# Optimization experiments

Measured on AMD Instinct MI355X. Metric: run time of the kernel, lower is better.

## Reference

```python
import jax, jax.numpy as jnp
import numpy as np

D_MODEL = 1024
HEADS = 16
HEAD_DIM = D_MODEL // HEADS


def setup_inputs() -> dict:
    key = jax.random.key(0)
    k_x, k_q, k_k, k_v, k_o = jax.random.split(key, 5)
    x = jax.random.normal(k_x, (4, 2048, D_MODEL), dtype=jnp.float32)
    W_q = jax.random.normal(k_q, (D_MODEL, D_MODEL), dtype=jnp.float32)
    W_k = jax.random.normal(k_k, (D_MODEL, D_MODEL), dtype=jnp.float32)
    W_v = jax.random.normal(k_v, (D_MODEL, D_MODEL), dtype=jnp.float32)
    fc_out = jax.random.normal(k_o, (D_MODEL, D_MODEL), dtype=jnp.float32)
    return {"x": x, "W_q": W_q, "W_k": W_k, "W_v": W_v, "fc_out": fc_out}


def reference(x, W_q, W_k, W_v, fc_out):
    b, s, d = x.shape
    h, hd = HEADS, HEAD_DIM
    # Projections: [b, s, d]
    Q = x @ W_q
    K = x @ W_k
    V = x @ W_v
    # Split heads: [b, h, s, hd]
    Q = Q.reshape(b, s, h, hd).transpose(0, 2, 1, 3)
    K = K.reshape(b, s, h, hd).transpose(0, 2, 1, 3)
    V = V.reshape(b, s, h, hd).transpose(0, 2, 1, 3)
    # Scaled dot-product attention (softmax over key axis, per row)
    scores = jnp.einsum('bhqd,bhkd->bhqk', Q, K) / jnp.sqrt(jnp.float32(hd))
    attn = jax.nn.softmax(scores, axis=-1)
    head_out = jnp.einsum('bhqk,bhkd->bhqd', attn, V)
    # Concat heads back: [b, s, d]
    concat = head_out.transpose(0, 2, 1, 3).reshape(b, s, d)
    return concat @ fc_out
```

## Files before the change

### kernel.cpp

```cpp
#include <hip/hip_runtime.h>
#include <hip/hip_fp16.h>

#define BATCH   4
#define SEQ     2048
#define DM      1024
#define HEADS   16
#define HD      64
#define M_TOK   (BATCH * SEQ)
#define QK_LD   2048

#define QSCALE  0.1803368801111204f

typedef __attribute__((ext_vector_type(8)))  _Float16 half8;
typedef __attribute__((ext_vector_type(4)))  float    f32x4;
typedef __attribute__((ext_vector_type(16))) float    f32x16;

__device__ __forceinline__ unsigned short f2h(float x) {
    return __half_as_ushort(__float2half(x));
}
__device__ __forceinline__ float h2f(unsigned short u) {
    return __half2float(__ushort_as_half(u));
}
__device__ __forceinline__ float fast_exp2(float x) {
    float r; asm volatile("v_exp_f32 %0, %1" : "=v"(r) : "v"(x)); return r;
}
__device__ __forceinline__ unsigned int pk2(float a, float b) {
    __fp16 __attribute__((ext_vector_type(2))) h =
        __builtin_amdgcn_cvt_pkrtz(a, b);
    return __builtin_bit_cast(unsigned int, h);
}
__device__ __forceinline__ void dma16(const void* g, void* l) {
    __builtin_amdgcn_global_load_lds(
        (const __attribute__((address_space(1))) void*)g,
        (__attribute__((address_space(3))) void*)l, 16, 0, 0);
}

__global__ __launch_bounds__(256) void split_cast(
    const float* __restrict__ x, unsigned short* __restrict__ hi,
    unsigned short* __restrict__ lo)
{
    const int i = (blockIdx.x * 256 + threadIdx.x) * 8;
    float4 a = *(const float4*)(x + i);
    float4 b = *(const float4*)(x + i + 4);
    float v[8] = {a.x, a.y, a.z, a.w, b.x, b.y, b.z, b.w};
    unsigned short hb[8], lb[8];
#pragma unroll
    for (int j = 0; j < 8; ++j) {
        hb[j] = f2h(v[j]);
        lb[j] = f2h(v[j] - h2f(hb[j]));
    }
    *(float4*)(hi + i) = *(float4*)hb;
    *(float4*)(lo + i) = *(float4*)lb;
}

template<int SPLIT>
__global__ __launch_bounds__(256) void wtrans(
    const float* __restrict__ W, unsigned short* __restrict__ Th_out,
    unsigned short* __restrict__ Tl_out, float scale)
{
    __shared__ unsigned short Th[64][72];
    __shared__ unsigned short Tl[SPLIT ? 64 : 1][72];
    const int t  = threadIdx.x;
    const int n0 = blockIdx.x * 64, k0 = blockIdx.y * 64;
    const int kr = t >> 2, cg = (t & 3) << 4;
#pragma unroll
    for (int jj = 0; jj < 16; jj += 4) {
        float4 wv = *(const float4*)(W + (size_t)(k0 + kr) * DM + n0 + cg + jj);
        float vv[4] = {wv.x, wv.y, wv.z, wv.w};
#pragma unroll
        for (int j = 0; j < 4; ++j) {
            float v = vv[j] * scale;
            unsigned short h = f2h(v);
            Th[cg + jj + j][kr] = h;
            if (SPLIT) Tl[cg + jj + j][kr] = f2h(v - h2f(h));
        }
    }
    __syncthreads();
    const int nr = t >> 2, kg = (t & 3) << 4;
    size_t go = (size_t)(n0 + nr) * DM + k0 + kg;
    *(float4*)(Th_out + go)     = *(float4*)&Th[nr][kg];
    *(float4*)(Th_out + go + 8) = *(float4*)&Th[nr][kg + 8];
    if (SPLIT) {
        *(float4*)(Tl_out + go)     = *(float4*)&Tl[nr][kg];
        *(float4*)(Tl_out + go + 8) = *(float4*)&Tl[nr][kg + 8];
    }
}

template<int PASSES, int EPI>
__global__ __launch_bounds__(256, 2) void gemm_f16(
    const unsigned short* __restrict__ Ah, const unsigned short* __restrict__ Al,
    const unsigned short* __restrict__ Bh, const unsigned short* __restrict__ Bl,
    void* __restrict__ O0, void* __restrict__ O1, int M, int N, int K)
{
    __shared__ unsigned short As_h[128 * 32];
    __shared__ unsigned short Bs_h[128 * 32];
    __shared__ unsigned short As_l[PASSES == 3 ? 128 * 32 : 16];
    __shared__ unsigned short Bs_l[PASSES == 3 ? 128 * 32 : 16];

    const int t = threadIdx.x;
    const int w = t >> 6, lane = t & 63, quad = lane >> 4, l15 = lane & 15;
    const int wm = w >> 1, wn = w & 1;
    const int m0 = blockIdx.y * 128, n0 = blockIdx.x * 128;

    const int drow = w * 32 + (lane >> 2);
    const int dcol = (lane & 3) * 8;

    f32x4 acc[4][4];
#pragma unroll
    for (int mt = 0; mt < 4; ++mt)
#pragma unroll
        for (int nt = 0; nt < 4; ++nt)
#pragma unroll
            for (int r = 0; r < 4; ++r) acc[mt][nt][r] = 0.f;

    for (int k0 = 0; k0 < K; k0 += 32) {
        __syncthreads();
#pragma unroll
        for (int inst = 0; inst < 2; ++inst) {
            const size_t ga = (size_t)(m0 + drow + inst * 16) * K + k0 + dcol;
            const size_t gb = (size_t)(n0 + drow + inst * 16) * K + k0 + dcol;
            const int lo = (w * 32 + inst * 16) * 32;
            dma16(Ah + ga, &As_h[lo]);
            dma16(Bh + gb, &Bs_h[lo]);
            if (PASSES == 3) {
                dma16(Al + ga, &As_l[lo]);
                dma16(Bl + gb, &Bs_l[lo]);
            }
        }
        __syncthreads();

        half8 aH[4], bH[4], aL[4], bL[4];
#pragma unroll
        for (int mt = 0; mt < 4; ++mt) {
            const int row = wm * 64 + mt * 16 + l15;
            aH[mt] = *(const half8*)&As_h[row * 32 + quad * 8];
            if (PASSES == 3) aL[mt] = *(const half8*)&As_l[row * 32 + quad * 8];
        }
#pragma unroll
        for (int nt = 0; nt < 4; ++nt) {
            const int row = wn * 64 + nt * 16 + l15;
            bH[nt] = *(const half8*)&Bs_h[row * 32 + quad * 8];
            if (PASSES == 3) bL[nt] = *(const half8*)&Bs_l[row * 32 + quad * 8];
        }
#pragma unroll
        for (int mt = 0; mt < 4; ++mt)
#pragma unroll
            for (int nt = 0; nt < 4; ++nt) {
                acc[mt][nt] = __builtin_amdgcn_mfma_f32_16x16x32_f16(
                    aH[mt], bH[nt], acc[mt][nt], 0, 0, 0);
                if (PASSES == 3) {
                    acc[mt][nt] = __builtin_amdgcn_mfma_f32_16x16x32_f16(
                        aH[mt], bL[nt], acc[mt][nt], 0, 0, 0);
                    acc[mt][nt] = __builtin_amdgcn_mfma_f32_16x16x32_f16(
                        aL[mt], bH[nt], acc[mt][nt], 0, 0, 0);
                }
            }
    }

#pragma unroll
    for (int mt = 0; mt < 4; ++mt)
#pragma unroll
        for (int nt = 0; nt < 4; ++nt) {
            const int row0 = m0 + wm * 64 + mt * 16 + quad * 4;
            const int col  = n0 + wn * 64 + nt * 16 + l15;
            if (EPI == 0) {
#pragma unroll
                for (int r = 0; r < 4; ++r)
                    ((float*)O0)[(size_t)(row0 + r) * N + col] = acc[mt][nt][r];
            } else if (EPI == 1) {
#pragma unroll
                for (int r = 0; r < 4; ++r) {
                    float v = acc[mt][nt][r];
                    unsigned short h = f2h(v);
                    ((unsigned short*)O0)[(size_t)(row0 + r) * N + col] = h;
                    ((unsigned short*)O1)[(size_t)(row0 + r) * N + col] =
                        f2h(v - h2f(h));
                }
            } else if (EPI == 2) {
#pragma unroll
                for (int r = 0; r < 4; ++r)
                    ((unsigned short*)O0)[(size_t)(row0 + r) * N + col] =
                        f2h(acc[mt][nt][r]);
            } else {
                const int b = row0 >> 11, s = row0 & 2047;
                const int hh = col >> 6, d = col & 63;
                unsigned short vs[4];
#pragma unroll
                for (int r = 0; r < 4; ++r) vs[r] = f2h(acc[mt][nt][r]);
                *(ushort4*)((unsigned short*)O0 +
                            (((size_t)(b * HEADS + hh)) * HD + d) * SEQ + s) =
                    *(ushort4*)vs;
            }
        }
}

__global__ __launch_bounds__(256, 3) void attn_f16(
    const unsigned short* __restrict__ QKh,
    const unsigned short* __restrict__ QKl,
    const unsigned short* __restrict__ Vt,
    unsigned short* __restrict__ Oc)
{
    __shared__ unsigned short SM[18432];
    unsigned short* Qh_s = SM;
    unsigned short* Ql_s = SM + 9216;
    unsigned short* Ks   = SM;
    unsigned short* Ksl  = SM + 4608;
    unsigned short* Vs   = SM + 9216;

    const int t = threadIdx.x;
    const int w = t >> 6, lane = t & 63;
    const int g = lane >> 5, l31 = lane & 31;
    const int b = blockIdx.z, h = blockIdx.y, q0 = blockIdx.x * 128;

    const size_t row0   = (size_t)b * SEQ;
    const size_t qcol   = (size_t)h * HD;
    const size_t kcol   = 1024 + qcol;
    const size_t vtbase = ((size_t)(b * HEADS + h)) * HD * SEQ;

    {
        const int sr = t >> 1, sc = (t & 1) * 32;
        const size_t gq = (row0 + q0 + sr) * QK_LD + qcol + sc;
#pragma unroll
        for (int c = 0; c < 32; c += 8) {
            *(float4*)&Qh_s[sr * 72 + sc + c] = *(const float4*)(QKh + gq + c);
            *(float4*)&Ql_s[sr * 72 + sc + c] = *(const float4*)(QKl + gq + c);
        }
    }
    __syncthreads();

    half8 bQh[4], bQl[4];
    {
        const int qr = (w * 32 + l31) * 72;
#pragma unroll
        for (int ks = 0; ks < 4; ++ks) {
            bQh[ks] = *(const half8*)&Qh_s[qr + ks * 16 + g * 8];
            bQl[ks] = *(const half8*)&Ql_s[qr + ks * 16 + g * 8];
        }
    }

    f32x16 o_acc[2];
#pragma unroll
    for (int mt = 0; mt < 2; ++mt)
#pragma unroll
        for (int r = 0; r < 16; ++r) o_acc[mt][r] = 0.f;
    float m_r = -3.0e38f, l_r = 0.f;

    const int sr = t >> 2, sc = (t & 3) * 16;

    for (int k0 = 0; k0 < SEQ; k0 += 64) {
        __syncthreads();
        {
            const size_t gk = (row0 + k0 + sr) * QK_LD + kcol + sc;
            *(float4*)&Ks [sr * 72 + sc]     = *(const float4*)(QKh + gk);
            *(float4*)&Ks [sr * 72 + sc + 8] = *(const float4*)(QKh + gk + 8);
            *(float4*)&Ksl[sr * 72 + sc]     = *(const float4*)(QKl + gk);
            *(float4*)&Ksl[sr * 72 + sc + 8] = *(const float4*)(QKl + gk + 8);
            const size_t gv = vtbase + (size_t)sr * SEQ + k0 + sc;
            *(float4*)&Vs[sr * 72 + sc]      = *(const float4*)(Vt + gv);
            *(float4*)&Vs[sr * 72 + sc + 8]  = *(const float4*)(Vt + gv + 8);
        }
        __syncthreads();

        f32x16 s[2];
#pragma unroll
        for (int kt = 0; kt < 2; ++kt)
#pragma unroll
            for (int r = 0; r < 16; ++r) s[kt][r] = 0.f;
#pragma unroll
        for (int kt = 0; kt < 2; ++kt)
#pragma unroll
            for (int ks = 0; ks < 4; ++ks) {
                const int aro = (kt * 32 + l31) * 72 + ks * 16 + g * 8;
                half8 aKh = *(const half8*)&Ks[aro];
                half8 aKl = *(const half8*)&Ksl[aro];
                s[kt] = __builtin_amdgcn_mfma_f32_32x32x16_f16(
                    aKh, bQh[ks], s[kt], 0, 0, 0);
                s[kt] = __builtin_amdgcn_mfma_f32_32x32x16_f16(
                    aKl, bQh[ks], s[kt], 0, 0, 0);
                s[kt] = __builtin_amdgcn_mfma_f32_32x32x16_f16(
                    aKh, bQl[ks], s[kt], 0, 0, 0);
            }

        float mx = s[0][0];
#pragma unroll
        for (int kt = 0; kt < 2; ++kt)
#pragma unroll
            for (int r = 0; r < 16; ++r) mx = fmaxf(mx, s[kt][r]);
        mx = fmaxf(mx, __shfl_xor(mx, 32));
        const float nm = fmaxf(m_r, mx);
        const float al = fast_exp2(m_r - nm);
        m_r = nm;
        float rs = 0.f;
#pragma unroll
        for (int kt = 0; kt < 2; ++kt)
#pragma unroll
            for (int r = 0; r < 16; ++r) {
                float pv = fast_exp2(s[kt][r] - nm);
                s[kt][r] = pv;
                rs += pv;
            }
        rs += __shfl_xor(rs, 32);
        l_r = l_r * al + rs;
#pragma unroll
        for (int mt = 0; mt < 2; ++mt)
#pragma unroll
            for (int r = 0; r < 16; ++r) o_acc[mt][r] *= al;

        half8 bP[4];
#pragma unroll
        for (int kt = 0; kt < 2; ++kt)
#pragma unroll
            for (int ksl = 0; ksl < 2; ++ksl) {
                const int base = ksl * 8;
                unsigned int lo0 = pk2(s[kt][base + 0], s[kt][base + 1]);
                unsigned int lo1 = pk2(s[kt][base + 2], s[kt][base + 3]);
                unsigned int hi0 = pk2(s[kt][base + 4], s[kt][base + 5]);
                unsigned int hi1 = pk2(s[kt][base + 6], s[kt][base + 7]);
                unsigned int s0 = g ? lo0 : hi0;
                unsigned int s1 = g ? lo1 : hi1;
                unsigned int r0 = (unsigned int)__shfl_xor((int)s0, 32);
                unsigned int r1 = (unsigned int)__shfl_xor((int)s1, 32);
                union { unsigned int u[4]; half8 hv; } u;
                u.u[0] = g ? r0 : lo0;
                u.u[1] = g ? r1 : lo1;
                u.u[2] = g ? hi0 : r0;
                u.u[3] = g ? hi1 : r1;
                bP[kt * 2 + ksl] = u.hv;
            }

#pragma unroll
        for (int mt = 0; mt < 2; ++mt)
#pragma unroll
            for (int kk = 0; kk < 4; ++kk) {
                half8 aV = *(const half8*)&Vs[(mt * 32 + l31) * 72 +
                                              kk * 16 + g * 8];
                o_acc[mt] = __builtin_amdgcn_mfma_f32_32x32x16_f16(
                    aV, bP[kk], o_acc[mt], 0, 0, 0);
            }
    }

    const float inv = 1.0f / l_r;
    unsigned short* orow = Oc + (row0 + q0 + w * 32 + l31) * DM + h * HD;
#pragma unroll
    for (int mt = 0; mt < 2; ++mt)
#pragma unroll
        for (int rq = 0; rq < 4; ++rq) {
            unsigned int w0 = pk2(o_acc[mt][rq * 4 + 0] * inv,
                                  o_acc[mt][rq * 4 + 1] * inv);
            unsigned int w1 = pk2(o_acc[mt][rq * 4 + 2] * inv,
                                  o_acc[mt][rq * 4 + 3] * inv);
            const int d0 = mt * 32 + rq * 8 + g * 4;
            uint2 pkd; pkd.x = w0; pkd.y = w1;
            *(uint2*)(orow + d0) = pkd;
        }
}

extern "C" void kernel_launch(void* const* d_in, const int* in_sizes, int n_in,
                              void* d_out, int out_size, void* d_ws, size_t ws_size,
                              hipStream_t stream) {
    const float* x  = (const float*)d_in[0];
    const float* Wq = (const float*)d_in[1];
    const float* Wk = (const float*)d_in[2];
    const float* Wv = (const float*)d_in[3];
    const float* Wo = (const float*)d_in[4];
    float* out = (float*)d_out;

    char* ws = (char*)d_ws;
    const size_t SZ_TOK = (size_t)M_TOK * DM * 2;
    const size_t SZ_W   = (size_t)DM * DM * 2;

    unsigned short* xh     = (unsigned short*)(ws);
    unsigned short* xl     = (unsigned short*)(ws + SZ_TOK);
    unsigned short* Wqkt_h = (unsigned short*)(ws + 2 * SZ_TOK);
    unsigned short* Wqkt_l = (unsigned short*)(ws + 2 * SZ_TOK + 2 * SZ_W);
    unsigned short* Wvt    = (unsigned short*)(ws + 2 * SZ_TOK + 4 * SZ_W);
    unsigned short* Wot    = (unsigned short*)(ws + 2 * SZ_TOK + 5 * SZ_W);
    unsigned short* QKh    = (unsigned short*)(ws + 2 * SZ_TOK + 6 * SZ_W);
    unsigned short* QKl    = (unsigned short*)(ws + 4 * SZ_TOK + 6 * SZ_W);
    unsigned short* Vt_    = (unsigned short*)(ws + 6 * SZ_TOK + 6 * SZ_W);
    unsigned short* concat = xh;

    dim3 blk(256);

    hipLaunchKernelGGL(split_cast, dim3(M_TOK * DM / (256 * 8)), blk, 0, stream,
                       x, xh, xl);
    dim3 wgrid(DM / 64, DM / 64);
    hipLaunchKernelGGL((wtrans<1>), wgrid, blk, 0, stream, Wq, Wqkt_h, Wqkt_l,
                       QSCALE);
    hipLaunchKernelGGL((wtrans<1>), wgrid, blk, 0, stream, Wk,
                       Wqkt_h + (size_t)DM * DM, Wqkt_l + (size_t)DM * DM, 1.0f);
    hipLaunchKernelGGL((wtrans<0>), wgrid, blk, 0, stream, Wv, Wvt, nullptr, 1.0f);
    hipLaunchKernelGGL((wtrans<0>), wgrid, blk, 0, stream, Wo, Wot, nullptr, 1.0f);

    dim3 gqk(QK_LD / 128, M_TOK / 128);
    hipLaunchKernelGGL((gemm_f16<3, 1>), gqk, blk, 0, stream,
                       xh, xl, Wqkt_h, Wqkt_l, QKh, QKl, M_TOK, QK_LD, DM);
    dim3 ggrid(DM / 128, M_TOK / 128);
    hipLaunchKernelGGL((gemm_f16<1, 3>), ggrid, blk, 0, stream,
                       xh, nullptr, Wvt, nullptr, Vt_, nullptr, M_TOK, DM, DM);

    dim3 agrid(SEQ / 128, HEADS, BATCH);
    hipLaunchKernelGGL(attn_f16, agrid, blk, 0, stream, QKh, QKl, Vt_, concat);

    hipLaunchKernelGGL((gemm_f16<1, 0>), ggrid, blk, 0, stream,
                       concat, nullptr, Wot, nullptr, out, nullptr, M_TOK, DM, DM);
}
```

Baseline: 485.9 us.

## Double-buffer GEMM and attention tiles with async DMA, enlarge attention query tile

The GEMM main loop now uses two shared-memory buffers and issues the async copy for the next K tile before computing on the current one, so global loads overlap MFMA work and one barrier per iteration is removed. The attention kernel also double-buffers its K/V tiles through async DMA with an XOR-swizzled layout instead of padded rows. Each block now processes 256 queries (two 128-query sub-tiles) so every K/V fragment read from shared memory feeds twice as many MFMAs. In exchange, register pressure and LDS use rise (occupancy bound lowered to 2) and the attention grid is halved, leaving fewer blocks to spread across CUs.

```diff
diff --git a/kernel.cpp b/kernel.cpp
--- a/kernel.cpp
+++ b/kernel.cpp
@@ -92,10 +92,10 @@
     const unsigned short* __restrict__ Bh, const unsigned short* __restrict__ Bl,
     void* __restrict__ O0, void* __restrict__ O1, int M, int N, int K)
 {
-    __shared__ unsigned short As_h[128 * 32];
-    __shared__ unsigned short Bs_h[128 * 32];
-    __shared__ unsigned short As_l[PASSES == 3 ? 128 * 32 : 16];
-    __shared__ unsigned short Bs_l[PASSES == 3 ? 128 * 32 : 16];
+    __shared__ unsigned short As_h[2][128 * 32];
+    __shared__ unsigned short Bs_h[2][128 * 32];
+    __shared__ unsigned short As_l[PASSES == 3 ? 2 : 1][PASSES == 3 ? 128 * 32 : 16];
+    __shared__ unsigned short Bs_l[PASSES == 3 ? 2 : 1][PASSES == 3 ? 128 * 32 : 16];
 
     const int t = threadIdx.x;
     const int w = t >> 6, lane = t & 63, quad = lane >> 4, l15 = lane & 15;
@@ -105,42 +105,48 @@
     const int drow = w * 32 + (lane >> 2);
     const int dcol = (lane & 3) * 8;
 
-    f32x4 acc[4][4];
-#pragma unroll
-    for (int mt = 0; mt < 4; ++mt)
-#pragma unroll
-        for (int nt = 0; nt < 4; ++nt)
-#pragma unroll
-            for (int r = 0; r < 4; ++r) acc[mt][nt][r] = 0.f;
-
-    for (int k0 = 0; k0 < K; k0 += 32) {
-        __syncthreads();
+    auto stage = [&](int buf, int k0) {
 #pragma unroll
         for (int inst = 0; inst < 2; ++inst) {
             const size_t ga = (size_t)(m0 + drow + inst * 16) * K + k0 + dcol;
             const size_t gb = (size_t)(n0 + drow + inst * 16) * K + k0 + dcol;
             const int lo = (w * 32 + inst * 16) * 32;
-            dma16(Ah + ga, &As_h[lo]);
-            dma16(Bh + gb, &Bs_h[lo]);
+            dma16(Ah + ga, &As_h[buf][lo]);
+            dma16(Bh + gb, &Bs_h[buf][lo]);
             if (PASSES == 3) {
-                dma16(Al + ga, &As_l[lo]);
-                dma16(Bl + gb, &Bs_l[lo]);
-            }
-        }
+                dma16(Al + ga, &As_l[buf][lo]);
+                dma16(Bl + gb, &Bs_l[buf][lo]);
+            }
+        }
+    };
+
+    f32x4 acc[4][4];
+#pragma unroll
+    for (int mt = 0; mt < 4; ++mt)
+#pragma unroll
+        for (int nt = 0; nt < 4; ++nt)
+#pragma unroll
+            for (int r = 0; r < 4; ++r) acc[mt][nt][r] = 0.f;
+
+    const int NIT = K >> 5;
+    stage(0, 0);
+    for (int it = 0; it < NIT; ++it) {
         __syncthreads();
+        const int cur = it & 1;
+        if (it + 1 < NIT) stage(cur ^ 1, (it + 1) * 32);
 
         half8 aH[4], bH[4], aL[4], bL[4];
 #pragma unroll
         for (int mt = 0; mt < 4; ++mt) {
             const int row = wm * 64 + mt * 16 + l15;
-            aH[mt] = *(const half8*)&As_h[row * 32 + quad * 8];
-            if (PASSES == 3) aL[mt] = *(const half8*)&As_l[row * 32 + quad * 8];
+            aH[mt] = *(const half8*)&As_h[cur][row * 32 + quad * 8];
+            if (PASSES == 3) aL[mt] = *(const half8*)&As_l[cur][row * 32 + quad * 8];
         }
 #pragma unroll
         for (int nt = 0; nt < 4; ++nt) {
             const int row = wn * 64 + nt * 16 + l15;
-            bH[nt] = *(const half8*)&Bs_h[row * 32 + quad * 8];
-            if (PASSES == 3) bL[nt] = *(const half8*)&Bs_l[row * 32 + quad * 8];
+            bH[nt] = *(const half8*)&Bs_h[cur][row * 32 + quad * 8];
+            if (PASSES == 3) bL[nt] = *(const half8*)&Bs_l[cur][row * 32 + quad * 8];
         }
 #pragma unroll
         for (int mt = 0; mt < 4; ++mt)
@@ -194,165 +200,177 @@
         }
 }
 
-__global__ __launch_bounds__(256, 3) void attn_f16(
+__global__ __launch_bounds__(256, 2) void attn_f16(
     const unsigned short* __restrict__ QKh,
     const unsigned short* __restrict__ QKl,
     const unsigned short* __restrict__ Vt,
     unsigned short* __restrict__ Oc)
 {
-    __shared__ unsigned short SM[18432];
-    unsigned short* Qh_s = SM;
-    unsigned short* Ql_s = SM + 9216;
-    unsigned short* Ks   = SM;
-    unsigned short* Ksl  = SM + 4608;
-    unsigned short* Vs   = SM + 9216;
+    __shared__ unsigned short SM[2][3 * 4096];
 
     const int t = threadIdx.x;
     const int w = t >> 6, lane = t & 63;
     const int g = lane >> 5, l31 = lane & 31;
-    const int b = blockIdx.z, h = blockIdx.y, q0 = blockIdx.x * 128;
+    const int b = blockIdx.z, h = blockIdx.y, q0 = blockIdx.x * 256;
 
     const size_t row0   = (size_t)b * SEQ;
     const size_t qcol   = (size_t)h * HD;
     const size_t kcol   = 1024 + qcol;
     const size_t vtbase = ((size_t)(b * HEADS + h)) * HD * SEQ;
 
-    {
-        const int sr = t >> 1, sc = (t & 1) * 32;
-        const size_t gq = (row0 + q0 + sr) * QK_LD + qcol + sc;
-#pragma unroll
-        for (int c = 0; c < 32; c += 8) {
-            *(float4*)&Qh_s[sr * 72 + sc + c] = *(const float4*)(QKh + gq + c);
-            *(float4*)&Ql_s[sr * 72 + sc + c] = *(const float4*)(QKl + gq + c);
-        }
-    }
-    __syncthreads();
-
-    half8 bQh[4], bQl[4];
-    {
-        const int qr = (w * 32 + l31) * 72;
+    const int rl  = lane >> 3;
+    const int sw8 = ((lane & 7) ^ (rl & 7)) * 8;
+    const int x7  = l31 & 7;
+
+    auto stage = [&](int buf, int k0) {
+#pragma unroll
+        for (int inst = 0; inst < 2; ++inst) {
+            const int r8 = w * 16 + inst * 8;
+            const size_t gk = (row0 + k0 + r8 + rl) * QK_LD + kcol + sw8;
+            const int lo = r8 * 64;
+            dma16(QKh + gk, &SM[buf][lo]);
+            dma16(QKl + gk, &SM[buf][4096 + lo]);
+            const size_t gv = vtbase + (size_t)(r8 + rl) * SEQ + k0 + sw8;
+            dma16(Vt + gv, &SM[buf][8192 + lo]);
+        }
+    };
+
+    half8 bQh[2][4], bQl[2][4];
+#pragma unroll
+    for (int qs = 0; qs < 2; ++qs) {
+        const size_t qr = (row0 + q0 + qs * 128 + w * 32 + l31) * QK_LD + qcol;
 #pragma unroll
         for (int ks = 0; ks < 4; ++ks) {
-            bQh[ks] = *(const half8*)&Qh_s[qr + ks * 16 + g * 8];
-            bQl[ks] = *(const half8*)&Ql_s[qr + ks * 16 + g * 8];
-        }
-    }
-
-    f32x16 o_acc[2];
-#pragma unroll
-    for (int mt = 0; mt < 2; ++mt)
-#pragma unroll
-        for (int r = 0; r < 16; ++r) o_acc[mt][r] = 0.f;
-    float m_r = -3.0e38f, l_r = 0.f;
-
-    const int sr = t >> 2, sc = (t & 3) * 16;
-
-    for (int k0 = 0; k0 < SEQ; k0 += 64) {
+            bQh[qs][ks] = *(const half8*)(QKh + qr + ks * 16 + g * 8);
+            bQl[qs][ks] = *(const half8*)(QKl + qr + ks * 16 + g * 8);
+        }
+    }
+
+    f32x16 o_acc[2][2];
+#pragma unroll
+    for (int qs = 0; qs < 2; ++qs)
+#pragma unroll
+        for (int mt = 0; mt < 2; ++mt)
+#pragma unroll
+            for (int r = 0; r < 16; ++r) o_acc[qs][mt][r] = 0.f;
+    float m_r[2] = {-3.0e38f, -3.0e38f}, l_r[2] = {0.f, 0.f};
+
+    stage(0, 0);
+    const int NIT = SEQ / 64;
+    for (int it = 0; it < NIT; ++it) {
         __syncthreads();
-        {
-            const size_t gk = (row0 + k0 + sr) * QK_LD + kcol + sc;
-            *(float4*)&Ks [sr * 72 + sc]     = *(const float4*)(QKh + gk);
-            *(float4*)&Ks [sr * 72 + sc + 8] = *(const float4*)(QKh + gk + 8);
-            *(float4*)&Ksl[sr * 72 + sc]     = *(const float4*)(QKl + gk);
-            *(float4*)&Ksl[sr * 72 + sc + 8] = *(const float4*)(QKl + gk + 8);
-            const size_t gv = vtbase + (size_t)sr * SEQ + k0 + sc;
-            *(float4*)&Vs[sr * 72 + sc]      = *(const float4*)(Vt + gv);
-            *(float4*)&Vs[sr * 72 + sc + 8]  = *(const float4*)(Vt + gv + 8);
-        }
-        __syncthreads();
-
-        f32x16 s[2];
+        const int cur = it & 1;
+        if (it + 1 < NIT) stage(cur ^ 1, (it + 1) * 64);
+        const unsigned short* Ks  = &SM[cur][0];
+        const unsigned short* Ksl = &SM[cur][4096];
+        const unsigned short* Vs  = &SM[cur][8192];
+
+        f32x16 s[2][2];
+#pragma unroll
+        for (int qs = 0; qs < 2; ++qs)
+#pragma unroll
+            for (int kt = 0; kt < 2; ++kt)
+#pragma unroll
+                for (int r = 0; r < 16; ++r) s[qs][kt][r] = 0.f;
 #pragma unroll
         for (int kt = 0; kt < 2; ++kt)
 #pragma unroll
-            for (int r = 0; r < 16; ++r) s[kt][r] = 0.f;
-#pragma unroll
-        for (int kt = 0; kt < 2; ++kt)
-#pragma unroll
             for (int ks = 0; ks < 4; ++ks) {
-                const int aro = (kt * 32 + l31) * 72 + ks * 16 + g * 8;
-                half8 aKh = *(const half8*)&Ks[aro];
-                half8 aKl = *(const half8*)&Ksl[aro];
-                s[kt] = __builtin_amdgcn_mfma_f32_32x32x16_f16(
-                    aKh, bQh[ks], s[kt], 0, 0, 0);
-                s[kt] = __builtin_amdgcn_mfma_f32_32x32x16_f16(
-                    aKl, bQh[ks], s[kt], 0, 0, 0);
-                s[kt] = __builtin_amdgcn_mfma_f32_32x32x16_f16(
-                    aKh, bQl[ks], s[kt], 0, 0, 0);
-            }
-
-        float mx = s[0][0];
-#pragma unroll
-        for (int kt = 0; kt < 2; ++kt)
-#pragma unroll
-            for (int r = 0; r < 16; ++r) mx = fmaxf(mx, s[kt][r]);
-        mx = fmaxf(mx, __shfl_xor(mx, 32));
-        const float nm = fmaxf(m_r, mx);
-        const float al = fast_exp2(m_r - nm);
-        m_r = nm;
-        float rs = 0.f;
-#pragma unroll
-        for (int kt = 0; kt < 2; ++kt)
-#pragma unroll
-            for (int r = 0; r < 16; ++r) {
-                float pv = fast_exp2(s[kt][r] - nm);
-                s[kt][r] = pv;
-                rs += pv;
-            }
-        rs += __shfl_xor(rs, 32);
-        l_r = l_r * al + rs;
+                const int off = (kt * 32 + l31) * 64 + (((ks * 2 + g) ^ x7) * 8);
+                half8 aKh = *(const half8*)&Ks[off];
+                half8 aKl = *(const half8*)&Ksl[off];
+#pragma unroll
+                for (int qs = 0; qs < 2; ++qs) {
+                    s[qs][kt] = __builtin_amdgcn_mfma_f32_32x32x16_f16(
+                        aKh, bQh[qs][ks], s[qs][kt], 0, 0, 0);
+                    s[qs][kt] = __builtin_amdgcn_mfma_f32_32x32x16_f16(
+                        aKl, bQh[qs][ks], s[qs][kt], 0, 0, 0);
+                    s[qs][kt] = __builtin_amdgcn_mfma_f32_32x32x16_f16(
+                        aKh, bQl[qs][ks], s[qs][kt], 0, 0, 0);
+                }
+            }
+
+        half8 bP[2][4];
+#pragma unroll
+        for (int qs = 0; qs < 2; ++qs) {
+            float mx = s[qs][0][0];
+#pragma unroll
+            for (int kt = 0; kt < 2; ++kt)
+#pragma unroll
+                for (int r = 0; r < 16; ++r) mx = fmaxf(mx, s[qs][kt][r]);
+            mx = fmaxf(mx, __shfl_xor(mx, 32));
+            const float nm = fmaxf(m_r[qs], mx);
+            const float al = fast_exp2(m_r[qs] - nm);
+            m_r[qs] = nm;
+            float rs = 0.f;
+#pragma unroll
+            for (int kt = 0; kt < 2; ++kt)
+#pragma unroll
+                for (int r = 0; r < 16; ++r) {
+                    float pv = fast_exp2(s[qs][kt][r] - nm);
+                    s[qs][kt][r] = pv;
+                    rs += pv;
+                }
+            rs += __shfl_xor(rs, 32);
+            l_r[qs] = l_r[qs] * al + rs;
+#pragma unroll
+            for (int mt = 0; mt < 2; ++mt)
+#pragma unroll
+                for (int r = 0; r < 16; ++r) o_acc[qs][mt][r] *= al;
+
+#pragma unroll
+            for (int kt = 0; kt < 2; ++kt)
+#pragma unroll
+                for (int ksl = 0; ksl < 2; ++ksl) {
+                    const int base = ksl * 8;
+                    unsigned int lo0 = pk2(s[qs][kt][base + 0], s[qs][kt][base + 1]);
+                    unsigned int lo1 = pk2(s[qs][kt][base + 2], s[qs][kt][base + 3]);
+                    unsigned int hi0 = pk2(s[qs][kt][base + 4], s[qs][kt][base + 5]);
+                    unsigned int hi1 = pk2(s[qs][kt][base + 6], s[qs][kt][base + 7]);
+                    unsigned int s0 = g ? lo0 : hi0;
+                    unsigned int s1 = g ? lo1 : hi1;
+                    unsigned int r0 = (unsigned int)__shfl_xor((int)s0, 32);
+                    unsigned int r1 = (unsigned int)__shfl_xor((int)s1, 32);
+                    union { unsigned int u[4]; half8 hv; } u;
+                    u.u[0] = g ? r0 : lo0;
+                    u.u[1] = g ? r1 : lo1;
+                    u.u[2] = g ? hi0 : r0;
+                    u.u[3] = g ? hi1 : r1;
+                    bP[qs][kt * 2 + ksl] = u.hv;
+                }
+        }
+
 #pragma unroll
         for (int mt = 0; mt < 2; ++mt)
 #pragma unroll
-            for (int r = 0; r < 16; ++r) o_acc[mt][r] *= al;
-
-        half8 bP[4];
-#pragma unroll
-        for (int kt = 0; kt < 2; ++kt)
-#pragma unroll
-            for (int ksl = 0; ksl < 2; ++ksl) {
-                const int base = ksl * 8;
-                unsigned int lo0 = pk2(s[kt][base + 0], s[kt][base + 1]);
-                unsigned int lo1 = pk2(s[kt][base + 2], s[kt][base + 3]);
-                unsigned int hi0 = pk2(s[kt][base + 4], s[kt][base + 5]);
-                unsigned int hi1 = pk2(s[kt][base + 6], s[kt][base + 7]);
-                unsigned int s0 = g ? lo0 : hi0;
-                unsigned int s1 = g ? lo1 : hi1;
-                unsigned int r0 = (unsigned int)__shfl_xor((int)s0, 32);
-                unsigned int r1 = (unsigned int)__shfl_xor((int)s1, 32);
-                union { unsigned int u[4]; half8 hv; } u;
-                u.u[0] = g ? r0 : lo0;
-                u.u[1] = g ? r1 : lo1;
-                u.u[2] = g ? hi0 : r0;
-                u.u[3] = g ? hi1 : r1;
-                bP[kt * 2 + ksl] = u.hv;
-            }
-
+            for (int kk = 0; kk < 4; ++kk) {
+                const int off = (mt * 32 + l31) * 64 + (((kk * 2 + g) ^ x7) * 8);
+                half8 aV = *(const half8*)&Vs[off];
+#pragma unroll
+                for (int qs = 0; qs < 2; ++qs)
+                    o_acc[qs][mt] = __builtin_amdgcn_mfma_f32_32x32x16_f16(
+                        aV, bP[qs][kk], o_acc[qs][mt], 0, 0, 0);
+            }
+    }
+
+#pragma unroll
+    for (int qs = 0; qs < 2; ++qs) {
+        const float inv = 1.0f / l_r[qs];
+        unsigned short* orow =
+            Oc + (row0 + q0 + qs * 128 + w * 32 + l31) * DM + h * HD;
 #pragma unroll
         for (int mt = 0; mt < 2; ++mt)
 #pragma unroll
-            for (int kk = 0; kk < 4; ++kk) {
-                half8 aV = *(const half8*)&Vs[(mt * 32 + l31) * 72 +
-                                              kk * 16 + g * 8];
-                o_acc[mt] = __builtin_amdgcn_mfma_f32_32x32x16_f16(
-                    aV, bP[kk], o_acc[mt], 0, 0, 0);
-            }
-    }
-
-    const float inv = 1.0f / l_r;
-    unsigned short* orow = Oc + (row0 + q0 + w * 32 + l31) * DM + h * HD;
-#pragma unroll
-    for (int mt = 0; mt < 2; ++mt)
-#pragma unroll
-        for (int rq = 0; rq < 4; ++rq) {
-            unsigned int w0 = pk2(o_acc[mt][rq * 4 + 0] * inv,
-                                  o_acc[mt][rq * 4 + 1] * inv);
-            unsigned int w1 = pk2(o_acc[mt][rq * 4 + 2] * inv,
-                                  o_acc[mt][rq * 4 + 3] * inv);
-            const int d0 = mt * 32 + rq * 8 + g * 4;
-            uint2 pkd; pkd.x = w0; pkd.y = w1;
-            *(uint2*)(orow + d0) = pkd;
-        }
+            for (int rq = 0; rq < 4; ++rq) {
+                unsigned int w0 = pk2(o_acc[qs][mt][rq * 4 + 0] * inv,
+                                      o_acc[qs][mt][rq * 4 + 1] * inv);
+                unsigned int w1 = pk2(o_acc[qs][mt][rq * 4 + 2] * inv,
+                                      o_acc[qs][mt][rq * 4 + 3] * inv);
+                const int d0 = mt * 32 + rq * 8 + g * 4;
+                uint2 pkd; pkd.x = w0; pkd.y = w1;
+                *(uint2*)(orow + d0) = pkd;
+            }
+    }
 }
 
 extern "C" void kernel_launch(void* const* d_in, const int* in_sizes, int n_in,
@@ -399,7 +417,7 @@
     hipLaunchKernelGGL((gemm_f16<1, 3>), ggrid, blk, 0, stream,
                        xh, nullptr, Wvt, nullptr, Vt_, nullptr, M_TOK, DM, DM);
 
-    dim3 agrid(SEQ / 128, HEADS, BATCH);
+    dim3 agrid(SEQ / 256, HEADS, BATCH);
     hipLaunchKernelGGL(attn_f16, agrid, blk, 0, stream, QKh, QKl, Vt_, concat);
 
     hipLaunchKernelGGL((gemm_f16<1, 0>), ggrid, blk, 0, stream,
```

Measured after the change: 433.0 us. 10.9% less time.
